# Kernel tuning notes

Hardware: AMD Instinct MI355X
Metric: run time of the kernel (lower is better)

Reference implementation:

```python
import jax, jax.numpy as jnp
import numpy as np

EPS = 1e-6
WINDOW = 1024  # config.sliding_window; mask: causal AND (q_idx - kv_idx < WINDOW)


def rms_norm(x, w=None):
    y = x * jax.lax.rsqrt(jnp.mean(jnp.square(x), axis=-1, keepdims=True) + EPS)
    return y * w if w is not None else y


def rotate_half(x):
    x1, x2 = jnp.split(x, 2, axis=-1)
    return jnp.concatenate([-x2, x1], axis=-1)


def apply_rope(x, cos, sin):
    # x: [B,S,H,D], cos/sin: [B,S,D] -> unsqueeze head dim (rotary_dim == D, x_pass empty)
    cos = cos[:, :, None, :]
    sin = sin[:, :, None, :]
    return x * cos + rotate_half(x) * sin


def setup_inputs() -> dict:
    key = jax.random.key(0)
    ks = jax.random.split(key, 8)
    B, S, HID, NH, NKV, D = 1, 2048, 2560, 8, 4, 256
    scale = 0.02
    hidden_states = jax.random.normal(ks[0], (B, S, HID), dtype=jnp.float32)
    wq = jax.random.normal(ks[1], (HID, NH * D), dtype=jnp.float32) * scale
    wk = jax.random.normal(ks[2], (HID, NKV * D), dtype=jnp.float32) * scale
    wv = jax.random.normal(ks[3], (HID, NKV * D), dtype=jnp.float32) * scale
    wo = jax.random.normal(ks[4], (NH * D, HID), dtype=jnp.float32) * scale
    q_norm_w = jnp.ones((D,), dtype=jnp.float32)
    k_norm_w = jnp.ones((D,), dtype=jnp.float32)
    # standard RoPE tables, rotary_dim = head_dim
    pos = jnp.arange(S, dtype=jnp.float32)
    inv_freq = 1.0 / (10000.0 ** (jnp.arange(0, D, 2, dtype=jnp.float32) / D))
    freqs = pos[:, None] * inv_freq[None, :]           # [S, D/2]
    emb = jnp.concatenate([freqs, freqs], axis=-1)     # [S, D]
    cos = jnp.cos(emb)[None]                           # [1, S, D]
    sin = jnp.sin(emb)[None]
    return dict(hidden_states=hidden_states, cos=cos, sin=sin,
                wq=wq, wk=wk, wv=wv, wo=wo,
                q_norm_w=q_norm_w, k_norm_w=k_norm_w)


def reference(hidden_states, cos, sin, wq, wk, wv, wo, q_norm_w, k_norm_w):
    B, S, _ = hidden_states.shape
    D = q_norm_w.shape[0]
    # projections -> [B,S,H,D]
    q = (hidden_states @ wq).reshape(B, S, -1, D)
    k = (hidden_states @ wk).reshape(B, S, -1, D)
    v = (hidden_states @ wv).reshape(B, S, -1, D)
    # QK-norm then RoPE (v gets non-affine RMSNorm)
    q = apply_rope(rms_norm(q, q_norm_w), cos, sin)
    k = apply_rope(rms_norm(k, k_norm_w), cos, sin)
    v = rms_norm(v)
    NH, NKV = q.shape[2], k.shape[2]
    rep = NH // NKV  # GQA: repeat KV heads
    k = jnp.repeat(k, rep, axis=2)
    v = jnp.repeat(v, rep, axis=2)
    # attention with scale=1.0 (QK-norm replaces 1/sqrt(d))
    scores = jnp.einsum('bqhd,bkhd->bhqk', q, k)
    qi = jnp.arange(S)[:, None]
    ki = jnp.arange(S)[None, :]
    mask = (ki <= qi) & (qi - ki < WINDOW)  # causal sliding window
    scores = jnp.where(mask[None, None], scores, -jnp.inf)
    attn = jax.nn.softmax(scores, axis=-1)
    out = jnp.einsum('bhqk,bkhd->bqhd', attn, v).reshape(B, S, -1)
    return out @ wo
```

## Files before the change

### kernel.cpp

```cpp
#include <hip/hip_runtime.h>
#include <hip/hip_bf16.h>
#include <math.h>

#define S_LEN 2048
#define HID 2560
#define NH 8
#define NKV 4
#define HD 256
#define WINDOW 1024

typedef short short8 __attribute__((ext_vector_type(8)));
typedef short short4_t __attribute__((ext_vector_type(4)));
typedef float f32x4 __attribute__((ext_vector_type(4)));
typedef float float4_t __attribute__((ext_vector_type(4)));

__device__ __forceinline__ short bf16_rne(float x) {
  unsigned u = __float_as_uint(x);
  return (short)((u + 0x7FFFu + ((u >> 16) & 1u)) >> 16);
}
__device__ __forceinline__ void split2(float x, short &h, short &l) {
  unsigned u = __float_as_uint(x);
  unsigned hb = (u + 0x7FFFu + ((u >> 16) & 1u)) & 0xFFFF0000u;
  h = (short)(hb >> 16);
  float r = x - __uint_as_float(hb);
  l = bf16_rne(r);
}

#define SWZ(g, r) ((((g) ^ ((r) & 7))) * 8)
__global__ __launch_bounds__(256, 3)
void gemm_presplit(const short* __restrict__ Ah, const short* __restrict__ Al,
                   const short* __restrict__ Bh, const short* __restrict__ Bl,
                   float* __restrict__ C, int M, int N, int K) {
  __shared__ short Ahs[64][64], Als[64][64];
  __shared__ short Bhs[128][64], Bls[128][64];
  const int tid = threadIdx.x;
  const int wv = tid >> 6, lane = tid & 63;
  const int wm = (wv >> 1) * 32, wn = (wv & 1) * 64;
  const int quad = lane >> 4, col = lane & 15;
  const int m0 = blockIdx.y * 64, n0 = blockIdx.x * 128;
  const int srow = tid >> 2, sg = tid & 3;

  f32x4 acc[2][4];
#pragma unroll
  for (int i = 0; i < 2; i++)
#pragma unroll
    for (int j = 0; j < 4; j++) acc[i][j] = (f32x4){0.f, 0.f, 0.f, 0.f};

  for (int k0 = 0; k0 < K; k0 += 64) {
#pragma unroll
    for (int gg = 0; gg < 2; gg++) {
      int g = sg + gg * 4;
      size_t go = (size_t)(m0 + srow) * K + k0 + g * 8;
      *reinterpret_cast<short8*>(&Ahs[srow][SWZ(g, srow)]) =
          *reinterpret_cast<const short8*>(Ah + go);
      *reinterpret_cast<short8*>(&Als[srow][SWZ(g, srow)]) =
          *reinterpret_cast<const short8*>(Al + go);
    }
#pragma unroll
    for (int rr = 0; rr < 2; rr++) {
      int row = srow + rr * 64;
#pragma unroll
      for (int gg = 0; gg < 2; gg++) {
        int g = sg + gg * 4;
        size_t go = (size_t)(n0 + row) * K + k0 + g * 8;
        *reinterpret_cast<short8*>(&Bhs[row][SWZ(g, row)]) =
            *reinterpret_cast<const short8*>(Bh + go);
        *reinterpret_cast<short8*>(&Bls[row][SWZ(g, row)]) =
            *reinterpret_cast<const short8*>(Bl + go);
      }
    }
    __syncthreads();
#pragma unroll
    for (int ks = 0; ks < 2; ks++) {
      const int g = ks * 4 + quad;
      short8 afh[2], afl[2], bfh[4], bfl[4];
#pragma unroll
      for (int i = 0; i < 2; i++) {
        int ar = wm + i * 16 + col;
        afh[i] = *reinterpret_cast<const short8*>(&Ahs[ar][SWZ(g, ar)]);
        afl[i] = *reinterpret_cast<const short8*>(&Als[ar][SWZ(g, ar)]);
      }
#pragma unroll
      for (int j = 0; j < 4; j++) {
        int br = wn + j * 16 + col;
        bfh[j] = *reinterpret_cast<const short8*>(&Bhs[br][SWZ(g, br)]);
        bfl[j] = *reinterpret_cast<const short8*>(&Bls[br][SWZ(g, br)]);
      }
#pragma unroll
      for (int i = 0; i < 2; i++)
#pragma unroll
        for (int j = 0; j < 4; j++) {
          acc[i][j] = __builtin_amdgcn_mfma_f32_16x16x32_bf16(afh[i], bfh[j], acc[i][j], 0, 0, 0);
          acc[i][j] = __builtin_amdgcn_mfma_f32_16x16x32_bf16(afh[i], bfl[j], acc[i][j], 0, 0, 0);
          acc[i][j] = __builtin_amdgcn_mfma_f32_16x16x32_bf16(afl[i], bfh[j], acc[i][j], 0, 0, 0);
        }
    }
    __syncthreads();
  }
#pragma unroll
  for (int i = 0; i < 2; i++)
#pragma unroll
    for (int j = 0; j < 4; j++)
#pragma unroll
      for (int r = 0; r < 4; r++)
        C[(size_t)(m0 + wm + i * 16 + quad * 4 + r) * N + n0 + wn + j * 16 + col] =
            acc[i][j][r];
}

__global__ __launch_bounds__(256)
void split_kernel(const float* __restrict__ in, short* __restrict__ oh,
                  short* __restrict__ ol, int n4) {
  int i = blockIdx.x * 256 + threadIdx.x;
  if (i >= n4) return;
  float4_t v = reinterpret_cast<const float4_t*>(in)[i];
  short4_t h, l;
#pragma unroll
  for (int e = 0; e < 4; e++) {
    short hh, ll;
    split2(v[e], hh, ll);
    h[e] = hh; l[e] = ll;
  }
  reinterpret_cast<short4_t*>(oh)[i] = h;
  reinterpret_cast<short4_t*>(ol)[i] = l;
}

__global__ __launch_bounds__(256)
void wsplitT_kernel(const float* __restrict__ W, short* __restrict__ WTh,
                    short* __restrict__ WTl, int KW, int NW, int n_ofs) {
  __shared__ float T[64][65];
  const int k0 = blockIdx.x * 64, n0 = blockIdx.y * 64;
  const int tid = threadIdx.x;
  const int r = tid >> 4, c4 = (tid & 15) * 4;
#pragma unroll
  for (int p = 0; p < 4; p++) {
    float4_t v = *reinterpret_cast<const float4_t*>(
        &W[(size_t)(k0 + r + p * 16) * NW + n0 + c4]);
#pragma unroll
    for (int e = 0; e < 4; e++) T[r + p * 16][c4 + e] = v[e];
  }
  __syncthreads();
  const int n_loc = tid >> 2, kg = (tid & 3) * 16;
  short8 hv[2], lv[2];
#pragma unroll
  for (int e = 0; e < 16; e++) {
    short hh, ll;
    split2(T[kg + e][n_loc], hh, ll);
    hv[e >> 3][e & 7] = hh;
    lv[e >> 3][e & 7] = ll;
  }
  size_t base = (size_t)(n_ofs + n0 + n_loc) * KW + k0 + kg;
  *reinterpret_cast<short8*>(WTh + base) = hv[0];
  *reinterpret_cast<short8*>(WTh + base + 8) = hv[1];
  *reinterpret_cast<short8*>(WTl + base) = lv[0];
  *reinterpret_cast<short8*>(WTl + base + 8) = lv[1];
}

struct GemmSmem {
  short Ah[128][32], Al[128][32], Bh[128][32], Bl[128][32];
};
__device__ __forceinline__ void gemm_body(GemmSmem* sm, const float* __restrict__ A,
                                          const float* __restrict__ B,
                                          float* __restrict__ C, int M, int N,
                                          int K, int m0, int n0) {
  const int tid = threadIdx.x;
  const int wave = tid >> 6, lane = tid & 63;
  const int wm = (wave >> 1) * 64, wn = (wave & 1) * 64;
  const int m_in = lane & 15, kgrp = lane >> 4;
  const int bn = tid & 127;
  const int bk0 = (tid >> 7) * 16;
  f32x4 acc[4][4];
#pragma unroll
  for (int i = 0; i < 4; i++)
#pragma unroll
    for (int j = 0; j < 4; j++) acc[i][j] = (f32x4){0.f, 0.f, 0.f, 0.f};
  for (int k0 = 0; k0 < K; k0 += 32) {
#pragma unroll
    for (int i = 0; i < 4; i++) {
      int f = tid + i * 256;
      int m = f >> 3, c4 = (f & 7) << 2;
      float4_t av = *reinterpret_cast<const float4_t*>(
          &A[(size_t)(m0 + m) * K + (k0 + c4)]);
      short4_t hv, lv;
#pragma unroll
      for (int e = 0; e < 4; e++) {
        short h, l;
        split2(av[e], h, l);
        hv[e] = h; lv[e] = l;
      }
      *reinterpret_cast<short4_t*>(&sm->Ah[m][c4]) = hv;
      *reinterpret_cast<short4_t*>(&sm->Al[m][c4]) = lv;
    }
    {
      const float* bp = &B[(size_t)(k0 + bk0) * N + (n0 + bn)];
      float vals[16];
#pragma unroll
      for (int kk = 0; kk < 16; kk++) vals[kk] = bp[(size_t)kk * N];
#pragma unroll
      for (int c = 0; c < 4; c++) {
        short4_t hv, lv;
#pragma unroll
        for (int e = 0; e < 4; e++) {
          short h, l;
          split2(vals[c * 4 + e], h, l);
          hv[e] = h; lv[e] = l;
        }
        *reinterpret_cast<short4_t*>(&sm->Bh[bn][bk0 + c * 4]) = hv;
        *reinterpret_cast<short4_t*>(&sm->Bl[bn][bk0 + c * 4]) = lv;
      }
    }
    __syncthreads();
    short8 ah[4], al[4], bh[4], bl[4];
#pragma unroll
    for (int i = 0; i < 4; i++) {
      ah[i] = *reinterpret_cast<const short8*>(&sm->Ah[wm + i * 16 + m_in][kgrp * 8]);
      al[i] = *reinterpret_cast<const short8*>(&sm->Al[wm + i * 16 + m_in][kgrp * 8]);
    }
#pragma unroll
    for (int j = 0; j < 4; j++) {
      bh[j] = *reinterpret_cast<const short8*>(&sm->Bh[wn + j * 16 + m_in][kgrp * 8]);
      bl[j] = *reinterpret_cast<const short8*>(&sm->Bl[wn + j * 16 + m_in][kgrp * 8]);
    }
#pragma unroll
    for (int i = 0; i < 4; i++)
#pragma unroll
      for (int j = 0; j < 4; j++) {
        acc[i][j] = __builtin_amdgcn_mfma_f32_16x16x32_bf16(ah[i], bh[j], acc[i][j], 0, 0, 0);
        acc[i][j] = __builtin_amdgcn_mfma_f32_16x16x32_bf16(ah[i], bl[j], acc[i][j], 0, 0, 0);
        acc[i][j] = __builtin_amdgcn_mfma_f32_16x16x32_bf16(al[i], bh[j], acc[i][j], 0, 0, 0);
      }
    __syncthreads();
  }
#pragma unroll
  for (int i = 0; i < 4; i++)
#pragma unroll
    for (int j = 0; j < 4; j++)
#pragma unroll
      for (int r = 0; r < 4; r++)
        C[(size_t)(m0 + wm + i * 16 + kgrp * 4 + r) * N + n0 + wn + j * 16 + m_in] =
            acc[i][j][r];
}
__global__ __launch_bounds__(256)
void gemm_mfma(const float* __restrict__ A, const float* __restrict__ B,
               float* __restrict__ C, int M, int N, int K) {
  __shared__ GemmSmem sm;
  gemm_body(&sm, A, B, C, M, N, K, blockIdx.y * 128, blockIdx.x * 128);
}
__global__ __launch_bounds__(256)
void gemm_mfma_kv(const float* __restrict__ A, const float* __restrict__ B0,
                  const float* __restrict__ B1, float* __restrict__ C0,
                  float* __restrict__ C1, int M, int N, int K) {
  __shared__ GemmSmem sm;
  const int nb = N / 128;
  const int half = blockIdx.x >= nb;
  gemm_body(&sm, A, half ? B1 : B0, half ? C1 : C0, M, N, K,
            blockIdx.y * 128, (blockIdx.x - half * nb) * 128);
}

__global__ __launch_bounds__(256)
void qnorm_kernel(float* __restrict__ io, int rs, const float* __restrict__ w,
                  const float* __restrict__ cosb, const float* __restrict__ sinb) {
  const int sq = blockIdx.x / NH;
  const int h = blockIdx.x % NH;
  const int d = threadIdx.x;
  const size_t idx = (size_t)sq * rs + h * HD + d;
  float x = io[idx];
  float v = x * x;
#pragma unroll
  for (int off = 32; off; off >>= 1) v += __shfl_down(v, off);
  __shared__ float red[4];
  __shared__ float sscale;
  __shared__ float nb[HD];
  if ((d & 63) == 0) red[d >> 6] = v;
  __syncthreads();
  if (d == 0)
    sscale = rsqrtf((red[0] + red[1] + red[2] + red[3]) * (1.0f / HD) + 1e-6f);
  __syncthreads();
  float n = x * sscale * w[d];
  nb[d] = n;
  __syncthreads();
  float other = (d < HD / 2) ? -nb[d + HD / 2] : nb[d - HD / 2];
  io[idx] = n * cosb[(size_t)sq * HD + d] + other * sinb[(size_t)sq * HD + d];
}

__global__ __launch_bounds__(256)
void knorm_split_kernel(const float* __restrict__ in, int rs,
                        short* __restrict__ kh, short* __restrict__ kl,
                        const float* __restrict__ w, const float* __restrict__ cosb,
                        const float* __restrict__ sinb) {
  const int sq = blockIdx.x / NKV;
  const int h = blockIdx.x % NKV;
  const int d = threadIdx.x;
  float x = in[(size_t)sq * rs + h * HD + d];
  float v = x * x;
#pragma unroll
  for (int off = 32; off; off >>= 1) v += __shfl_down(v, off);
  __shared__ float red[4];
  __shared__ float sscale;
  __shared__ float nb[HD];
  if ((d & 63) == 0) red[d >> 6] = v;
  __syncthreads();
  if (d == 0)
    sscale = rsqrtf((red[0] + red[1] + red[2] + red[3]) * (1.0f / HD) + 1e-6f);
  __syncthreads();
  float n = x * sscale * w[d];
  nb[d] = n;
  __syncthreads();
  float other = (d < HD / 2) ? -nb[d + HD / 2] : nb[d - HD / 2];
  n = n * cosb[(size_t)sq * HD + d] + other * sinb[(size_t)sq * HD + d];
  short hh, ll;
  split2(n, hh, ll);
  kh[((size_t)sq * NKV + h) * HD + d] = hh;
  kl[((size_t)sq * NKV + h) * HD + d] = ll;
}

__global__ __launch_bounds__(256)
void vnormT_kernel(const float* __restrict__ in, int rs, short* __restrict__ vtb) {
  const int sq = blockIdx.x / NKV;
  const int h = blockIdx.x % NKV;
  const int d = threadIdx.x;
  float x = in[(size_t)sq * rs + h * HD + d];
  float v = x * x;
#pragma unroll
  for (int off = 32; off; off >>= 1) v += __shfl_down(v, off);
  __shared__ float red[4];
  __shared__ float sscale;
  if ((d & 63) == 0) red[d >> 6] = v;
  __syncthreads();
  if (d == 0)
    sscale = rsqrtf((red[0] + red[1] + red[2] + red[3]) * (1.0f / HD) + 1e-6f);
  __syncthreads();
  vtb[((size_t)h * HD + d) * S_LEN + sq] = bf16_rne(x * sscale);
}

__global__ __launch_bounds__(256, 2)
void flash_attn2(const float* __restrict__ qn, int qrs,
                 const short* __restrict__ kh, const short* __restrict__ kl,
                 const short* __restrict__ vtb, float* __restrict__ oA,
                 float* __restrict__ oB, float* __restrict__ mlA,
                 float* __restrict__ mlB) {
  __shared__ short Kh[32][264], Kl[32][264];
  __shared__ short Vb[256][40];
  __shared__ short Ps[64][40];
  const int qt = blockIdx.x, h = blockIdx.y, sp = blockIdx.z;
  const int kvh = h >> 1;
  const int q0 = qt * 64;
  const int tid = threadIdx.x;
  const int w = tid >> 6, lane = tid & 63;
  const int quad = lane >> 4, col = lane & 15;
  float* oOut = sp ? oB : oA;
  float* mlOut = sp ? mlB : mlA;
  short8 qh[8], ql[8];
  {
    const float* qrow = qn + (size_t)(q0 + w * 16 + col) * qrs + h * HD;
#pragma unroll
    for (int s8 = 0; s8 < 8; s8++) {
      int d0 = s8 * 32 + quad * 8;
      float4_t a = *reinterpret_cast<const float4_t*>(qrow + d0);
      float4_t b = *reinterpret_cast<const float4_t*>(qrow + d0 + 4);
#pragma unroll
      for (int e = 0; e < 4; e++) {
        short hh, ll;
        split2(a[e], hh, ll);
        qh[s8][e] = hh; ql[s8][e] = ll;
        split2(b[e], hh, ll);
        qh[s8][4 + e] = hh; ql[s8][4 + e] = ll;
      }
    }
  }
  f32x4 o[16];
#pragma unroll
  for (int i = 0; i < 16; i++) o[i] = (f32x4){0.f, 0.f, 0.f, 0.f};
  float m_r[4] = {-INFINITY, -INFINITY, -INFINITY, -INFINITY};
  float l_r[4] = {0.f, 0.f, 0.f, 0.f};
  const int lo_t = (q0 > 1023) ? ((q0 - 1023) >> 5) : 0;
  const int hi_t = (q0 + 63) >> 5;
  const int halfn = (hi_t - lo_t + 2) >> 1;
  const int t0 = sp ? (lo_t + halfn) : lo_t;
  const int t1 = sp ? hi_t : (lo_t + halfn - 1);
  for (int kt = t0; kt <= t1; kt++) {
    const int kt0 = kt << 5;
    __syncthreads();
#pragma unroll
    for (int i = 0; i < 4; i++) {
      int idx = tid + i * 256;
      int row = idx >> 5, g = idx & 31;
      size_t gofs = ((size_t)(kt0 + row) * NKV + kvh) * HD + g * 8;
      *reinterpret_cast<short8*>(&Kh[row][g * 8]) =
          *reinterpret_cast<const short8*>(kh + gofs);
      *reinterpret_cast<short8*>(&Kl[row][g * 8]) =
          *reinterpret_cast<const short8*>(kl + gofs);
    }
#pragma unroll
    for (int i = 0; i < 4; i++) {
      int idx = tid + i * 256;
      int d = idx >> 2, g = idx & 3;
      *reinterpret_cast<short8*>(&Vb[d][g * 8]) = *reinterpret_cast<const short8*>(
          vtb + ((size_t)kvh * HD + d) * S_LEN + kt0 + g * 8);
    }
    __syncthreads();
    f32x4 sc[2];
    sc[0] = (f32x4){0.f, 0.f, 0.f, 0.f};
    sc[1] = (f32x4){0.f, 0.f, 0.f, 0.f};
#pragma unroll
    for (int s8 = 0; s8 < 8; s8++) {
#pragma unroll
      for (int nt = 0; nt < 2; nt++) {
        const short8 bh = *reinterpret_cast<const short8*>(
            &Kh[nt * 16 + col][s8 * 32 + quad * 8]);
        const short8 bl = *reinterpret_cast<const short8*>(
            &Kl[nt * 16 + col][s8 * 32 + quad * 8]);
        sc[nt] = __builtin_amdgcn_mfma_f32_16x16x32_bf16(qh[s8], bh, sc[nt], 0, 0, 0);
        sc[nt] = __builtin_amdgcn_mfma_f32_16x16x32_bf16(qh[s8], bl, sc[nt], 0, 0, 0);
        sc[nt] = __builtin_amdgcn_mfma_f32_16x16x32_bf16(ql[s8], bh, sc[nt], 0, 0, 0);
      }
    }
#pragma unroll
    for (int r = 0; r < 4; r++) {
      const int q_abs = q0 + w * 16 + quad * 4 + r;
#pragma unroll
      for (int nt = 0; nt < 2; nt++) {
        int k_abs = kt0 + nt * 16 + col;
        bool valid = (k_abs <= q_abs) && (q_abs - k_abs < WINDOW);
        if (!valid) sc[nt][r] = -INFINITY;
      }
      float mx = fmaxf(sc[0][r], sc[1][r]);
      mx = fmaxf(mx, __shfl_xor(mx, 1));
      mx = fmaxf(mx, __shfl_xor(mx, 2));
      mx = fmaxf(mx, __shfl_xor(mx, 4));
      mx = fmaxf(mx, __shfl_xor(mx, 8));
      float mn = fmaxf(m_r[r], mx);
      float alpha = (mn == -INFINITY) ? 1.f : __expf(m_r[r] - mn);
      m_r[r] = mn;
      float rsum = 0.f;
#pragma unroll
      for (int nt = 0; nt < 2; nt++) {
        float s = sc[nt][r];
        float e = (s == -INFINITY) ? 0.f : __expf(s - mn);
        rsum += e;
        Ps[w * 16 + quad * 4 + r][nt * 16 + col] = bf16_rne(e);
      }
      rsum += __shfl_xor(rsum, 1);
      rsum += __shfl_xor(rsum, 2);
      rsum += __shfl_xor(rsum, 4);
      rsum += __shfl_xor(rsum, 8);
      l_r[r] = l_r[r] * alpha + rsum;
#pragma unroll
      for (int nt2 = 0; nt2 < 16; nt2++) o[nt2][r] *= alpha;
    }
    __syncthreads();
    {
      const short8 pa = *reinterpret_cast<const short8*>(&Ps[w * 16 + col][quad * 8]);
#pragma unroll
      for (int nt = 0; nt < 16; nt++) {
        const short8 vb = *reinterpret_cast<const short8*>(&Vb[nt * 16 + col][quad * 8]);
        o[nt] = __builtin_amdgcn_mfma_f32_16x16x32_bf16(pa, vb, o[nt], 0, 0, 0);
      }
    }
  }
#pragma unroll
  for (int r = 0; r < 4; r++) {
    const int row = q0 + w * 16 + quad * 4 + r;
    const size_t base = ((size_t)row * NH + h) * HD;
#pragma unroll
    for (int nt = 0; nt < 16; nt++) oOut[base + nt * 16 + col] = o[nt][r];
    if (col == 0) {
      mlOut[((size_t)row * NH + h) * 2] = m_r[r];
      mlOut[((size_t)row * NH + h) * 2 + 1] = l_r[r];
    }
  }
}

__global__ __launch_bounds__(256)
void combine_kernel(const float* __restrict__ oA, const float* __restrict__ oB,
                    const float* __restrict__ mlA, const float* __restrict__ mlB,
                    float* __restrict__ ctxf, short* __restrict__ ctxh,
                    short* __restrict__ ctxl, int mode) {
  const int idx = blockIdx.x;
  const int d = threadIdx.x;
  const float mA = mlA[(size_t)idx * 2], lA = mlA[(size_t)idx * 2 + 1];
  const float mB = mlB[(size_t)idx * 2], lB = mlB[(size_t)idx * 2 + 1];
  const float m = fmaxf(mA, mB);
  const float eA = (mA == -INFINITY) ? 0.f : __expf(mA - m);
  const float eB = (mB == -INFINITY) ? 0.f : __expf(mB - m);
  const float inv = 1.0f / (eA * lA + eB * lB);
  const size_t b = (size_t)idx * HD + d;
  float v = (eA * oA[b] + eB * oB[b]) * inv;
  if (mode == 0) {
    ctxf[b] = v;
  } else {
    short hh, ll;
    split2(v, hh, ll);
    ctxh[b] = hh;
    ctxl[b] = ll;
  }
}

extern "C" void kernel_launch(void* const* d_in, const int* in_sizes, int n_in,
                              void* d_out, int out_size, void* d_ws, size_t ws_size,
                              hipStream_t stream) {
  const float* hs   = (const float*)d_in[0];
  const float* cosb = (const float*)d_in[1];
  const float* sinb = (const float*)d_in[2];
  const float* wq   = (const float*)d_in[3];
  const float* wk   = (const float*)d_in[4];
  const float* wv   = (const float*)d_in[5];
  const float* wo   = (const float*)d_in[6];
  const float* qw   = (const float*)d_in[7];
  const float* kw   = (const float*)d_in[8];
  dim3 blk(256);

  const size_t szAh   = (size_t)S_LEN * HID * 2;
  const size_t szQKVT = (size_t)4096 * HID * 2;
  const size_t szWoT  = (size_t)HID * 2048 * 2;
  const size_t szCqkv = (size_t)S_LEN * 4096 * 4;
  const size_t szKh   = (size_t)S_LEN * NKV * HD * 2;
  const size_t szMl   = (size_t)S_LEN * NH * 2 * 4;
  const size_t NEED = 256 + 2 * szAh + 2 * szQKVT + 2 * szWoT + szCqkv +
                      3 * szKh + 2 * szMl + 4096;

  if (ws_size >= NEED) {
    char* p = (char*)d_ws + 256;
    short* Ah     = (short*)p;              p += szAh;
    short* Al     = (short*)p;              p += szAh;
    short* qkvTh  = (short*)p;              p += szQKVT;
    short* qkvTl  = (short*)p;              p += szQKVT;
    short* woTh   = (short*)p;              p += szWoT;
    short* woTl   = (short*)p;              p += szWoT;
    float* Cqkv   = (float*)p;              p += szCqkv;
    short* kh     = (short*)p;              p += szKh;
    short* kl     = (short*)p;              p += szKh;
    short* vtb    = (short*)p;              p += szKh;
    float* mlA    = (float*)p;              p += szMl;
    float* mlB    = (float*)p;              p += szMl;
    float* oA     = (float*)Ah;
    float* oB     = (float*)d_out;
    short* ctxh   = qkvTh;
    short* ctxl   = qkvTh + (size_t)S_LEN * NH * HD;

    split_kernel<<<(S_LEN * HID / 4 + 255) / 256, blk, 0, stream>>>(
        hs, Ah, Al, S_LEN * HID / 4);
    wsplitT_kernel<<<dim3(HID / 64, 2048 / 64), blk, 0, stream>>>(
        wq, qkvTh, qkvTl, HID, 2048, 0);
    wsplitT_kernel<<<dim3(HID / 64, 1024 / 64), blk, 0, stream>>>(
        wk, qkvTh, qkvTl, HID, 1024, 2048);
    wsplitT_kernel<<<dim3(HID / 64, 1024 / 64), blk, 0, stream>>>(
        wv, qkvTh, qkvTl, HID, 1024, 3072);
    wsplitT_kernel<<<dim3(2048 / 64, HID / 64), blk, 0, stream>>>(
        wo, woTh, woTl, 2048, HID, 0);
    gemm_presplit<<<dim3(4096 / 128, S_LEN / 64), blk, 0, stream>>>(
        Ah, Al, qkvTh, qkvTl, Cqkv, S_LEN, 4096, HID);
    qnorm_kernel<<<S_LEN * NH, blk, 0, stream>>>(Cqkv, 4096, qw, cosb, sinb);
    knorm_split_kernel<<<S_LEN * NKV, blk, 0, stream>>>(Cqkv + 2048, 4096, kh, kl,
                                                        kw, cosb, sinb);
    vnormT_kernel<<<S_LEN * NKV, blk, 0, stream>>>(Cqkv + 3072, 4096, vtb);
    flash_attn2<<<dim3(S_LEN / 64, NH, 2), blk, 0, stream>>>(
        Cqkv, 4096, kh, kl, vtb, oA, oB, mlA, mlB);
    combine_kernel<<<S_LEN * NH, blk, 0, stream>>>(oA, oB, mlA, mlB, nullptr,
                                                   ctxh, ctxl, 1);
    gemm_presplit<<<dim3(HID / 128, S_LEN / 64), blk, 0, stream>>>(
        ctxh, ctxl, woTh, woTl, (float*)d_out, S_LEN, HID, 2048);
  } else {
    float* qc  = (float*)((char*)d_ws + 256);
    float* Xk  = qc + (size_t)S_LEN * NH * HD;
    float* Xv  = Xk + (size_t)S_LEN * NKV * HD;
    float* oA  = Xk;
    short* kh  = (short*)(Xv + (size_t)S_LEN * NKV * HD);
    short* kl  = kh + (size_t)S_LEN * NKV * HD;
    short* vtb = kl + (size_t)S_LEN * NKV * HD;
    float* mlA = (float*)(vtb + (size_t)S_LEN * NKV * HD);
    float* mlB = mlA + (size_t)S_LEN * NH * 2;
    float* oB  = (float*)d_out;
    gemm_mfma_kv<<<dim3(16, S_LEN / 128), blk, 0, stream>>>(
        hs, wk, wv, Xk, Xv, S_LEN, NKV * HD, HID);
    knorm_split_kernel<<<S_LEN * NKV, blk, 0, stream>>>(Xk, NKV * HD, kh, kl,
                                                        kw, cosb, sinb);
    vnormT_kernel<<<S_LEN * NKV, blk, 0, stream>>>(Xv, NKV * HD, vtb);
    gemm_mfma<<<dim3((NH * HD) / 128, S_LEN / 128), blk, 0, stream>>>(
        hs, wq, qc, S_LEN, NH * HD, HID);
    qnorm_kernel<<<S_LEN * NH, blk, 0, stream>>>(qc, NH * HD, qw, cosb, sinb);
    flash_attn2<<<dim3(S_LEN / 64, NH, 2), blk, 0, stream>>>(
        qc, NH * HD, kh, kl, vtb, oA, oB, mlA, mlB);
    combine_kernel<<<S_LEN * NH, blk, 0, stream>>>(oA, oB, mlA, mlB, qc,
                                                   nullptr, nullptr, 0);
    gemm_mfma<<<dim3(HID / 128, S_LEN / 128), blk, 0, stream>>>(
        qc, wo, (float*)d_out, S_LEN, HID, NH * HD);
  }
}
```

Baseline: 503.7 us.

## Template split-bf16 GEMM precision per operand, swizzle attention LDS, drop fallback path

The presplit GEMM becomes a template over which low-order operand parts are used. The V projection drops the activation low part. The output projection takes a single-bf16 context, so combine now writes only the high bf16. The flash-attention kernel removes padded LDS rows in favour of XOR/rotate swizzles, raising occupancy hints to 3. The wsplitT store pattern is reorganised and the fp32 fallback path is deleted. These changes cut MFMA count and LDS traffic but lower the precision of the V and output projections, which risks accuracy.

```diff
diff --git a/kernel.cpp b/kernel.cpp
--- a/kernel.cpp
+++ b/kernel.cpp
@@ -27,12 +27,17 @@
 }
 
 #define SWZ(g, r) ((((g) ^ ((r) & 7))) * 8)
+template <int MODE>
 __global__ __launch_bounds__(256, 3)
 void gemm_presplit(const short* __restrict__ Ah, const short* __restrict__ Al,
                    const short* __restrict__ Bh, const short* __restrict__ Bl,
-                   float* __restrict__ C, int M, int N, int K) {
-  __shared__ short Ahs[64][64], Als[64][64];
-  __shared__ short Bhs[128][64], Bls[128][64];
+                   float* __restrict__ C, int K, int ldc) {
+  constexpr bool USE_AL = (MODE & 1) != 0;
+  constexpr bool USE_BL = (MODE & 2) != 0;
+  __shared__ short Ahs[64][64];
+  __shared__ short Als[USE_AL ? 64 : 1][64];
+  __shared__ short Bhs[128][64];
+  __shared__ short Bls[USE_BL ? 128 : 1][64];
   const int tid = threadIdx.x;
   const int wv = tid >> 6, lane = tid & 63;
   const int wm = (wv >> 1) * 32, wn = (wv & 1) * 64;
@@ -53,8 +58,9 @@
       size_t go = (size_t)(m0 + srow) * K + k0 + g * 8;
       *reinterpret_cast<short8*>(&Ahs[srow][SWZ(g, srow)]) =
           *reinterpret_cast<const short8*>(Ah + go);
-      *reinterpret_cast<short8*>(&Als[srow][SWZ(g, srow)]) =
-          *reinterpret_cast<const short8*>(Al + go);
+      if (USE_AL)
+        *reinterpret_cast<short8*>(&Als[srow][SWZ(g, srow)]) =
+            *reinterpret_cast<const short8*>(Al + go);
     }
 #pragma unroll
     for (int rr = 0; rr < 2; rr++) {
@@ -65,8 +71,9 @@
         size_t go = (size_t)(n0 + row) * K + k0 + g * 8;
         *reinterpret_cast<short8*>(&Bhs[row][SWZ(g, row)]) =
             *reinterpret_cast<const short8*>(Bh + go);
-        *reinterpret_cast<short8*>(&Bls[row][SWZ(g, row)]) =
-            *reinterpret_cast<const short8*>(Bl + go);
+        if (USE_BL)
+          *reinterpret_cast<short8*>(&Bls[row][SWZ(g, row)]) =
+              *reinterpret_cast<const short8*>(Bl + go);
       }
     }
     __syncthreads();
@@ -78,21 +85,25 @@
       for (int i = 0; i < 2; i++) {
         int ar = wm + i * 16 + col;
         afh[i] = *reinterpret_cast<const short8*>(&Ahs[ar][SWZ(g, ar)]);
-        afl[i] = *reinterpret_cast<const short8*>(&Als[ar][SWZ(g, ar)]);
+        if (USE_AL)
+          afl[i] = *reinterpret_cast<const short8*>(&Als[ar][SWZ(g, ar)]);
       }
 #pragma unroll
       for (int j = 0; j < 4; j++) {
         int br = wn + j * 16 + col;
         bfh[j] = *reinterpret_cast<const short8*>(&Bhs[br][SWZ(g, br)]);
-        bfl[j] = *reinterpret_cast<const short8*>(&Bls[br][SWZ(g, br)]);
+        if (USE_BL)
+          bfl[j] = *reinterpret_cast<const short8*>(&Bls[br][SWZ(g, br)]);
       }
 #pragma unroll
       for (int i = 0; i < 2; i++)
 #pragma unroll
         for (int j = 0; j < 4; j++) {
           acc[i][j] = __builtin_amdgcn_mfma_f32_16x16x32_bf16(afh[i], bfh[j], acc[i][j], 0, 0, 0);
-          acc[i][j] = __builtin_amdgcn_mfma_f32_16x16x32_bf16(afh[i], bfl[j], acc[i][j], 0, 0, 0);
-          acc[i][j] = __builtin_amdgcn_mfma_f32_16x16x32_bf16(afl[i], bfh[j], acc[i][j], 0, 0, 0);
+          if (USE_BL)
+            acc[i][j] = __builtin_amdgcn_mfma_f32_16x16x32_bf16(afh[i], bfl[j], acc[i][j], 0, 0, 0);
+          if (USE_AL)
+            acc[i][j] = __builtin_amdgcn_mfma_f32_16x16x32_bf16(afl[i], bfh[j], acc[i][j], 0, 0, 0);
         }
     }
     __syncthreads();
@@ -103,7 +114,7 @@
     for (int j = 0; j < 4; j++)
 #pragma unroll
       for (int r = 0; r < 4; r++)
-        C[(size_t)(m0 + wm + i * 16 + quad * 4 + r) * N + n0 + wn + j * 16 + col] =
+        C[(size_t)(m0 + wm + i * 16 + quad * 4 + r) * ldc + n0 + wn + j * 16 + col] =
             acc[i][j][r];
 }
 
@@ -139,121 +150,21 @@
     for (int e = 0; e < 4; e++) T[r + p * 16][c4 + e] = v[e];
   }
   __syncthreads();
-  const int n_loc = tid >> 2, kg = (tid & 3) * 16;
-  short8 hv[2], lv[2];
-#pragma unroll
-  for (int e = 0; e < 16; e++) {
-    short hh, ll;
-    split2(T[kg + e][n_loc], hh, ll);
-    hv[e >> 3][e & 7] = hh;
-    lv[e >> 3][e & 7] = ll;
-  }
-  size_t base = (size_t)(n_ofs + n0 + n_loc) * KW + k0 + kg;
-  *reinterpret_cast<short8*>(WTh + base) = hv[0];
-  *reinterpret_cast<short8*>(WTh + base + 8) = hv[1];
-  *reinterpret_cast<short8*>(WTl + base) = lv[0];
-  *reinterpret_cast<short8*>(WTl + base + 8) = lv[1];
-}
-
-struct GemmSmem {
-  short Ah[128][32], Al[128][32], Bh[128][32], Bl[128][32];
-};
-__device__ __forceinline__ void gemm_body(GemmSmem* sm, const float* __restrict__ A,
-                                          const float* __restrict__ B,
-                                          float* __restrict__ C, int M, int N,
-                                          int K, int m0, int n0) {
-  const int tid = threadIdx.x;
-  const int wave = tid >> 6, lane = tid & 63;
-  const int wm = (wave >> 1) * 64, wn = (wave & 1) * 64;
-  const int m_in = lane & 15, kgrp = lane >> 4;
-  const int bn = tid & 127;
-  const int bk0 = (tid >> 7) * 16;
-  f32x4 acc[4][4];
-#pragma unroll
-  for (int i = 0; i < 4; i++)
-#pragma unroll
-    for (int j = 0; j < 4; j++) acc[i][j] = (f32x4){0.f, 0.f, 0.f, 0.f};
-  for (int k0 = 0; k0 < K; k0 += 32) {
-#pragma unroll
-    for (int i = 0; i < 4; i++) {
-      int f = tid + i * 256;
-      int m = f >> 3, c4 = (f & 7) << 2;
-      float4_t av = *reinterpret_cast<const float4_t*>(
-          &A[(size_t)(m0 + m) * K + (k0 + c4)]);
-      short4_t hv, lv;
-#pragma unroll
-      for (int e = 0; e < 4; e++) {
-        short h, l;
-        split2(av[e], h, l);
-        hv[e] = h; lv[e] = l;
-      }
-      *reinterpret_cast<short4_t*>(&sm->Ah[m][c4]) = hv;
-      *reinterpret_cast<short4_t*>(&sm->Al[m][c4]) = lv;
-    }
-    {
-      const float* bp = &B[(size_t)(k0 + bk0) * N + (n0 + bn)];
-      float vals[16];
-#pragma unroll
-      for (int kk = 0; kk < 16; kk++) vals[kk] = bp[(size_t)kk * N];
-#pragma unroll
-      for (int c = 0; c < 4; c++) {
-        short4_t hv, lv;
-#pragma unroll
-        for (int e = 0; e < 4; e++) {
-          short h, l;
-          split2(vals[c * 4 + e], h, l);
-          hv[e] = h; lv[e] = l;
-        }
-        *reinterpret_cast<short4_t*>(&sm->Bh[bn][bk0 + c * 4]) = hv;
-        *reinterpret_cast<short4_t*>(&sm->Bl[bn][bk0 + c * 4]) = lv;
-      }
-    }
-    __syncthreads();
-    short8 ah[4], al[4], bh[4], bl[4];
-#pragma unroll
-    for (int i = 0; i < 4; i++) {
-      ah[i] = *reinterpret_cast<const short8*>(&sm->Ah[wm + i * 16 + m_in][kgrp * 8]);
-      al[i] = *reinterpret_cast<const short8*>(&sm->Al[wm + i * 16 + m_in][kgrp * 8]);
-    }
-#pragma unroll
-    for (int j = 0; j < 4; j++) {
-      bh[j] = *reinterpret_cast<const short8*>(&sm->Bh[wn + j * 16 + m_in][kgrp * 8]);
-      bl[j] = *reinterpret_cast<const short8*>(&sm->Bl[wn + j * 16 + m_in][kgrp * 8]);
-    }
-#pragma unroll
-    for (int i = 0; i < 4; i++)
-#pragma unroll
-      for (int j = 0; j < 4; j++) {
-        acc[i][j] = __builtin_amdgcn_mfma_f32_16x16x32_bf16(ah[i], bh[j], acc[i][j], 0, 0, 0);
-        acc[i][j] = __builtin_amdgcn_mfma_f32_16x16x32_bf16(ah[i], bl[j], acc[i][j], 0, 0, 0);
-        acc[i][j] = __builtin_amdgcn_mfma_f32_16x16x32_bf16(al[i], bh[j], acc[i][j], 0, 0, 0);
-      }
-    __syncthreads();
-  }
-#pragma unroll
-  for (int i = 0; i < 4; i++)
-#pragma unroll
-    for (int j = 0; j < 4; j++)
-#pragma unroll
-      for (int r = 0; r < 4; r++)
-        C[(size_t)(m0 + wm + i * 16 + kgrp * 4 + r) * N + n0 + wn + j * 16 + m_in] =
-            acc[i][j][r];
-}
-__global__ __launch_bounds__(256)
-void gemm_mfma(const float* __restrict__ A, const float* __restrict__ B,
-               float* __restrict__ C, int M, int N, int K) {
-  __shared__ GemmSmem sm;
-  gemm_body(&sm, A, B, C, M, N, K, blockIdx.y * 128, blockIdx.x * 128);
-}
-__global__ __launch_bounds__(256)
-void gemm_mfma_kv(const float* __restrict__ A, const float* __restrict__ B0,
-                  const float* __restrict__ B1, float* __restrict__ C0,
-                  float* __restrict__ C1, int M, int N, int K) {
-  __shared__ GemmSmem sm;
-  const int nb = N / 128;
-  const int half = blockIdx.x >= nb;
-  gemm_body(&sm, A, half ? B1 : B0, half ? C1 : C0, M, N, K,
-            blockIdx.y * 128, (blockIdx.x - half * nb) * 128);
+  const int gk = tid & 7;
+#pragma unroll
+  for (int pass = 0; pass < 2; pass++) {
+    const int n_loc = (tid >> 3) + pass * 32;
+    short8 hv, lv;
+#pragma unroll
+    for (int e = 0; e < 8; e++) {
+      short hh, ll;
+      split2(T[gk * 8 + e][n_loc], hh, ll);
+      hv[e] = hh; lv[e] = ll;
+    }
+    size_t base = (size_t)(n_ofs + n0 + n_loc) * KW + k0 + gk * 8;
+    *reinterpret_cast<short8*>(WTh + base) = hv;
+    *reinterpret_cast<short8*>(WTl + base) = lv;
+  }
 }
 
 __global__ __launch_bounds__(256)
@@ -332,15 +243,17 @@
   vtb[((size_t)h * HD + d) * S_LEN + sq] = bf16_rne(x * sscale);
 }
 
-__global__ __launch_bounds__(256, 2)
+#define KSW(g, r) (((g) ^ ((r) & 7)) * 8)
+#define VSW(g, d) ((((g) + ((d) >> 1)) & 3) * 8)
+__global__ __launch_bounds__(256, 3)
 void flash_attn2(const float* __restrict__ qn, int qrs,
                  const short* __restrict__ kh, const short* __restrict__ kl,
                  const short* __restrict__ vtb, float* __restrict__ oA,
                  float* __restrict__ oB, float* __restrict__ mlA,
                  float* __restrict__ mlB) {
-  __shared__ short Kh[32][264], Kl[32][264];
-  __shared__ short Vb[256][40];
-  __shared__ short Ps[64][40];
+  __shared__ short Kh[32][256], Kl[32][256];
+  __shared__ short Vb[256][32];
+  __shared__ short Ps[64][32];
   const int qt = blockIdx.x, h = blockIdx.y, sp = blockIdx.z;
   const int kvh = h >> 1;
   const int q0 = qt * 64;
@@ -385,17 +298,18 @@
       int idx = tid + i * 256;
       int row = idx >> 5, g = idx & 31;
       size_t gofs = ((size_t)(kt0 + row) * NKV + kvh) * HD + g * 8;
-      *reinterpret_cast<short8*>(&Kh[row][g * 8]) =
+      *reinterpret_cast<short8*>(&Kh[row][KSW(g, row)]) =
           *reinterpret_cast<const short8*>(kh + gofs);
-      *reinterpret_cast<short8*>(&Kl[row][g * 8]) =
+      *reinterpret_cast<short8*>(&Kl[row][KSW(g, row)]) =
           *reinterpret_cast<const short8*>(kl + gofs);
     }
 #pragma unroll
     for (int i = 0; i < 4; i++) {
       int idx = tid + i * 256;
       int d = idx >> 2, g = idx & 3;
-      *reinterpret_cast<short8*>(&Vb[d][g * 8]) = *reinterpret_cast<const short8*>(
-          vtb + ((size_t)kvh * HD + d) * S_LEN + kt0 + g * 8);
+      *reinterpret_cast<short8*>(&Vb[d][VSW(g, d)]) =
+          *reinterpret_cast<const short8*>(
+              vtb + ((size_t)kvh * HD + d) * S_LEN + kt0 + g * 8);
     }
     __syncthreads();
     f32x4 sc[2];
@@ -405,10 +319,11 @@
     for (int s8 = 0; s8 < 8; s8++) {
 #pragma unroll
       for (int nt = 0; nt < 2; nt++) {
+        const int br = nt * 16 + col;
         const short8 bh = *reinterpret_cast<const short8*>(
-            &Kh[nt * 16 + col][s8 * 32 + quad * 8]);
+            &Kh[br][KSW(s8 * 4 + quad, br)]);
         const short8 bl = *reinterpret_cast<const short8*>(
-            &Kl[nt * 16 + col][s8 * 32 + quad * 8]);
+            &Kl[br][KSW(s8 * 4 + quad, br)]);
         sc[nt] = __builtin_amdgcn_mfma_f32_16x16x32_bf16(qh[s8], bh, sc[nt], 0, 0, 0);
         sc[nt] = __builtin_amdgcn_mfma_f32_16x16x32_bf16(qh[s8], bl, sc[nt], 0, 0, 0);
         sc[nt] = __builtin_amdgcn_mfma_f32_16x16x32_bf16(ql[s8], bh, sc[nt], 0, 0, 0);
@@ -417,6 +332,7 @@
 #pragma unroll
     for (int r = 0; r < 4; r++) {
       const int q_abs = q0 + w * 16 + quad * 4 + r;
+      const int prow = w * 16 + quad * 4 + r;
 #pragma unroll
       for (int nt = 0; nt < 2; nt++) {
         int k_abs = kt0 + nt * 16 + col;
@@ -437,7 +353,8 @@
         float s = sc[nt][r];
         float e = (s == -INFINITY) ? 0.f : __expf(s - mn);
         rsum += e;
-        Ps[w * 16 + quad * 4 + r][nt * 16 + col] = bf16_rne(e);
+        int ge = nt * 2 + (col >> 3);
+        Ps[prow][VSW(ge, prow) + (col & 7)] = bf16_rne(e);
       }
       rsum += __shfl_xor(rsum, 1);
       rsum += __shfl_xor(rsum, 2);
@@ -449,10 +366,12 @@
     }
     __syncthreads();
     {
-      const short8 pa = *reinterpret_cast<const short8*>(&Ps[w * 16 + col][quad * 8]);
+      const int prow = w * 16 + col;
+      const short8 pa = *reinterpret_cast<const short8*>(&Ps[prow][VSW(quad, prow)]);
 #pragma unroll
       for (int nt = 0; nt < 16; nt++) {
-        const short8 vb = *reinterpret_cast<const short8*>(&Vb[nt * 16 + col][quad * 8]);
+        const int vr = nt * 16 + col;
+        const short8 vb = *reinterpret_cast<const short8*>(&Vb[vr][VSW(quad, vr)]);
         o[nt] = __builtin_amdgcn_mfma_f32_16x16x32_bf16(pa, vb, o[nt], 0, 0, 0);
       }
     }
@@ -473,8 +392,7 @@
 __global__ __launch_bounds__(256)
 void combine_kernel(const float* __restrict__ oA, const float* __restrict__ oB,
                     const float* __restrict__ mlA, const float* __restrict__ mlB,
-                    float* __restrict__ ctxf, short* __restrict__ ctxh,
-                    short* __restrict__ ctxl, int mode) {
+                    short* __restrict__ ctxh) {
   const int idx = blockIdx.x;
   const int d = threadIdx.x;
   const float mA = mlA[(size_t)idx * 2], lA = mlA[(size_t)idx * 2 + 1];
@@ -484,15 +402,7 @@
   const float eB = (mB == -INFINITY) ? 0.f : __expf(mB - m);
   const float inv = 1.0f / (eA * lA + eB * lB);
   const size_t b = (size_t)idx * HD + d;
-  float v = (eA * oA[b] + eB * oB[b]) * inv;
-  if (mode == 0) {
-    ctxf[b] = v;
-  } else {
-    short hh, ll;
-    split2(v, hh, ll);
-    ctxh[b] = hh;
-    ctxl[b] = ll;
-  }
+  ctxh[b] = bf16_rne((eA * oA[b] + eB * oB[b]) * inv);
 }
 
 extern "C" void kernel_launch(void* const* d_in, const int* in_sizes, int n_in,
@@ -515,74 +425,46 @@
   const size_t szCqkv = (size_t)S_LEN * 4096 * 4;
   const size_t szKh   = (size_t)S_LEN * NKV * HD * 2;
   const size_t szMl   = (size_t)S_LEN * NH * 2 * 4;
-  const size_t NEED = 256 + 2 * szAh + 2 * szQKVT + 2 * szWoT + szCqkv +
-                      3 * szKh + 2 * szMl + 4096;
-
-  if (ws_size >= NEED) {
-    char* p = (char*)d_ws + 256;
-    short* Ah     = (short*)p;              p += szAh;
-    short* Al     = (short*)p;              p += szAh;
-    short* qkvTh  = (short*)p;              p += szQKVT;
-    short* qkvTl  = (short*)p;              p += szQKVT;
-    short* woTh   = (short*)p;              p += szWoT;
-    short* woTl   = (short*)p;              p += szWoT;
-    float* Cqkv   = (float*)p;              p += szCqkv;
-    short* kh     = (short*)p;              p += szKh;
-    short* kl     = (short*)p;              p += szKh;
-    short* vtb    = (short*)p;              p += szKh;
-    float* mlA    = (float*)p;              p += szMl;
-    float* mlB    = (float*)p;              p += szMl;
-    float* oA     = (float*)Ah;
-    float* oB     = (float*)d_out;
-    short* ctxh   = qkvTh;
-    short* ctxl   = qkvTh + (size_t)S_LEN * NH * HD;
-
-    split_kernel<<<(S_LEN * HID / 4 + 255) / 256, blk, 0, stream>>>(
-        hs, Ah, Al, S_LEN * HID / 4);
-    wsplitT_kernel<<<dim3(HID / 64, 2048 / 64), blk, 0, stream>>>(
-        wq, qkvTh, qkvTl, HID, 2048, 0);
-    wsplitT_kernel<<<dim3(HID / 64, 1024 / 64), blk, 0, stream>>>(
-        wk, qkvTh, qkvTl, HID, 1024, 2048);
-    wsplitT_kernel<<<dim3(HID / 64, 1024 / 64), blk, 0, stream>>>(
-        wv, qkvTh, qkvTl, HID, 1024, 3072);
-    wsplitT_kernel<<<dim3(2048 / 64, HID / 64), blk, 0, stream>>>(
-        wo, woTh, woTl, 2048, HID, 0);
-    gemm_presplit<<<dim3(4096 / 128, S_LEN / 64), blk, 0, stream>>>(
-        Ah, Al, qkvTh, qkvTl, Cqkv, S_LEN, 4096, HID);
-    qnorm_kernel<<<S_LEN * NH, blk, 0, stream>>>(Cqkv, 4096, qw, cosb, sinb);
-    knorm_split_kernel<<<S_LEN * NKV, blk, 0, stream>>>(Cqkv + 2048, 4096, kh, kl,
-                                                        kw, cosb, sinb);
-    vnormT_kernel<<<S_LEN * NKV, blk, 0, stream>>>(Cqkv + 3072, 4096, vtb);
-    flash_attn2<<<dim3(S_LEN / 64, NH, 2), blk, 0, stream>>>(
-        Cqkv, 4096, kh, kl, vtb, oA, oB, mlA, mlB);
-    combine_kernel<<<S_LEN * NH, blk, 0, stream>>>(oA, oB, mlA, mlB, nullptr,
-                                                   ctxh, ctxl, 1);
-    gemm_presplit<<<dim3(HID / 128, S_LEN / 64), blk, 0, stream>>>(
-        ctxh, ctxl, woTh, woTl, (float*)d_out, S_LEN, HID, 2048);
-  } else {
-    float* qc  = (float*)((char*)d_ws + 256);
-    float* Xk  = qc + (size_t)S_LEN * NH * HD;
-    float* Xv  = Xk + (size_t)S_LEN * NKV * HD;
-    float* oA  = Xk;
-    short* kh  = (short*)(Xv + (size_t)S_LEN * NKV * HD);
-    short* kl  = kh + (size_t)S_LEN * NKV * HD;
-    short* vtb = kl + (size_t)S_LEN * NKV * HD;
-    float* mlA = (float*)(vtb + (size_t)S_LEN * NKV * HD);
-    float* mlB = mlA + (size_t)S_LEN * NH * 2;
-    float* oB  = (float*)d_out;
-    gemm_mfma_kv<<<dim3(16, S_LEN / 128), blk, 0, stream>>>(
-        hs, wk, wv, Xk, Xv, S_LEN, NKV * HD, HID);
-    knorm_split_kernel<<<S_LEN * NKV, blk, 0, stream>>>(Xk, NKV * HD, kh, kl,
-                                                        kw, cosb, sinb);
-    vnormT_kernel<<<S_LEN * NKV, blk, 0, stream>>>(Xv, NKV * HD, vtb);
-    gemm_mfma<<<dim3((NH * HD) / 128, S_LEN / 128), blk, 0, stream>>>(
-        hs, wq, qc, S_LEN, NH * HD, HID);
-    qnorm_kernel<<<S_LEN * NH, blk, 0, stream>>>(qc, NH * HD, qw, cosb, sinb);
-    flash_attn2<<<dim3(S_LEN / 64, NH, 2), blk, 0, stream>>>(
-        qc, NH * HD, kh, kl, vtb, oA, oB, mlA, mlB);
-    combine_kernel<<<S_LEN * NH, blk, 0, stream>>>(oA, oB, mlA, mlB, qc,
-                                                   nullptr, nullptr, 0);
-    gemm_mfma<<<dim3(HID / 128, S_LEN / 128), blk, 0, stream>>>(
-        qc, wo, (float*)d_out, S_LEN, HID, NH * HD);
-  }
-}
+
+  char* p = (char*)d_ws + 256;
+  short* Ah    = (short*)p;  p += szAh;
+  short* Al    = (short*)p;  p += szAh;
+  short* qkvTh = (short*)p;  p += szQKVT;
+  short* qkvTl = (short*)p;  p += szQKVT;
+  short* woTh  = (short*)p;  p += szWoT;
+  short* woTl  = (short*)p;  p += szWoT;
+  float* Cqkv  = (float*)p;  p += szCqkv;
+  short* kh    = (short*)p;  p += szKh;
+  short* kl    = (short*)p;  p += szKh;
+  short* vtb   = (short*)p;  p += szKh;
+  float* mlA   = (float*)p;  p += szMl;
+  float* mlB   = (float*)p;  p += szMl;
+  float* oA    = (float*)Ah;
+  float* oB    = (float*)d_out;
+  short* ctxh  = qkvTh;
+
+  split_kernel<<<(S_LEN * HID / 4 + 255) / 256, blk, 0, stream>>>(
+      hs, Ah, Al, S_LEN * HID / 4);
+  wsplitT_kernel<<<dim3(HID / 64, 2048 / 64), blk, 0, stream>>>(
+      wq, qkvTh, qkvTl, HID, 2048, 0);
+  wsplitT_kernel<<<dim3(HID / 64, 1024 / 64), blk, 0, stream>>>(
+      wk, qkvTh, qkvTl, HID, 1024, 2048);
+  wsplitT_kernel<<<dim3(HID / 64, 1024 / 64), blk, 0, stream>>>(
+      wv, qkvTh, qkvTl, HID, 1024, 3072);
+  wsplitT_kernel<<<dim3(2048 / 64, HID / 64), blk, 0, stream>>>(
+      wo, woTh, woTl, 2048, HID, 0);
+  gemm_presplit<3><<<dim3(3072 / 128, S_LEN / 64), blk, 0, stream>>>(
+      Ah, Al, qkvTh, qkvTl, Cqkv, HID, 4096);
+  gemm_presplit<2><<<dim3(1024 / 128, S_LEN / 64), blk, 0, stream>>>(
+      Ah, Al, qkvTh + (size_t)3072 * HID, qkvTl + (size_t)3072 * HID,
+      Cqkv + 3072, HID, 4096);
+  qnorm_kernel<<<S_LEN * NH, blk, 0, stream>>>(Cqkv, 4096, qw, cosb, sinb);
+  knorm_split_kernel<<<S_LEN * NKV, blk, 0, stream>>>(Cqkv + 2048, 4096, kh, kl,
+                                                      kw, cosb, sinb);
+  vnormT_kernel<<<S_LEN * NKV, blk, 0, stream>>>(Cqkv + 3072, 4096, vtb);
+  flash_attn2<<<dim3(S_LEN / 64, NH, 2), blk, 0, stream>>>(
+      Cqkv, 4096, kh, kl, vtb, oA, oB, mlA, mlB);
+  combine_kernel<<<S_LEN * NH, blk, 0, stream>>>(oA, oB, mlA, mlB, ctxh);
+  gemm_presplit<2><<<dim3(HID / 128, S_LEN / 64), blk, 0, stream>>>(
+      ctxh, ctxh, woTh, woTl, (float*)d_out, 2048, HID);
+}
```

Result: slower. 604.6 us (+20.0%).
